# Optimization experiments

Measured on AMD Instinct MI355X. Metric: run time of the kernel, lower is better.

Reference implementation:

```python
import jax, jax.numpy as jnp
import numpy as np


def _coord(n):
    # grid-center coordinates in [-1, 1], matching make_coord
    r = 1.0 / n
    return -1.0 + r + 2.0 * r * jnp.arange(n, dtype=jnp.float32)


def setup_inputs() -> dict:
    key = jax.random.key(0)
    k1, k2, k3 = jax.random.split(key, 3)
    B, C, H, W = 4, 64, 128, 128
    n_feat = 64
    return {
        "x": jax.random.normal(k1, (B, C, H, W), jnp.float32),
        "W1": jax.random.normal(k2, (n_feat + 2, n_feat), jnp.float32) * 0.05,
        "b1": jnp.zeros((n_feat,), jnp.float32),
        "W2": jax.random.normal(k3, (n_feat, 3), jnp.float32) * 0.05,
        "b2": jnp.zeros((3,), jnp.float32),
        "out_size": 512,
    }


def reference(x, W1, b1, W2, b2, out_size):
    # radius == 1 -> F.unfold(x, 1, padding=0) is the identity, so x_unfold == x.
    B, C, H, W = x.shape
    Oh = Ow = out_size

    yc = _coord(Oh)  # [Oh] output-pixel-center y coords in [-1,1]
    xc = _coord(Ow)  # [Ow]

    # grid_sample(mode='nearest', align_corners=False): unnormalize then round
    # (nearbyint = round-half-to-even, matched by jnp.round). Coords are in
    # bounds, so clipping reproduces the in-range gather exactly.
    iy = jnp.clip(jnp.round(((yc + 1.0) * H - 1.0) * 0.5), 0, H - 1).astype(jnp.int32)
    ix = jnp.clip(jnp.round(((xc + 1.0) * W - 1.0) * 0.5), 0, W - 1).astype(jnp.int32)

    # nearest-neighbor gather of features: [B, C, Oh, Ow] -> [B, Oh, Ow, C]
    q_feat = jnp.transpose(x[:, :, iy, :][:, :, :, ix], (0, 2, 3, 1))

    # nearest input pixel-center coords (what grid-sampling in_coord returns)
    qy = -1.0 + (2.0 * iy.astype(jnp.float32) + 1.0) / H  # [Oh]
    qx = -1.0 + (2.0 * ix.astype(jnp.float32) + 1.0) / W  # [Ow]

    rel_y = (yc - qy) * H  # scaled by x.shape[-2]
    rel_x = (xc - qx) * W  # scaled by x.shape[-1]
    rel = jnp.stack(jnp.broadcast_arrays(rel_y[:, None], rel_x[None, :]), axis=-1)  # [Oh,Ow,2]

    inp = jnp.concatenate(
        [q_feat, jnp.broadcast_to(rel, (B, Oh, Ow, 2))], axis=-1
    )  # [B, Oh, Ow, C+2]

    h = jax.nn.relu(inp @ W1 + b1)   # [B, Oh, Ow, n_feat]
    pred = h @ W2 + b2               # [B, Oh, Ow, 3]
    return jnp.transpose(pred, (0, 3, 1, 2))  # [B, 3, Oh, Ow]
```

## Files before the change

kernel.cpp:

```cpp
#include <hip/hip_runtime.h>
#include <hip/hip_bf16.h>


#define PLANE (512 * 512)
#define PITCH 68

typedef __attribute__((ext_vector_type(8))) short  short8;
typedef __attribute__((ext_vector_type(4))) float  f32x4;

__device__ __forceinline__ short bf16_of(float f) {
    __hip_bfloat16 h = __float2bfloat16(f);
    return *reinterpret_cast<short*>(&h);
}

__global__ __launch_bounds__(512, 8) void mlp_interp_kernel(
    const float* __restrict__ x,
    const float* __restrict__ W1,
    const float* __restrict__ b1,
    const float* __restrict__ W2,
    const float* __restrict__ b2,
    float* __restrict__ out)
{
    __shared__ float fs[64][PITCH];

    const int tid = threadIdx.x;
    const int w   = tid >> 6;
    const int t   = tid & 63;

    const int blk  = blockIdx.x;
    const int lblk = blk & 1;
    const int k    = (blk >> 1) & 127;
    const int b    = blk >> 8;
    const int l0   = lblk * 64;

    {
        const int lane16 = t & 15;
        const int g      = t >> 4;
        const int mt     = w >> 1;
        const int nt0    = (w & 1) * 2;

        const float* xbase = x + (((size_t)(b * 64)) * 128 + k) * 128
                               + l0 + 16 * mt + lane16;
        short8 afrag[2];
        #pragma unroll
        for (int ks = 0; ks < 2; ++ks) {
            float tmp[8];
            #pragma unroll
            for (int i = 0; i < 8; ++i)
                tmp[i] = xbase[(size_t)(32 * ks + 8 * g + i) * 16384];
            #pragma unroll
            for (int i = 0; i < 8; ++i) afrag[ks][i] = bf16_of(tmp[i]);
        }

        #pragma unroll
        for (int ntp = 0; ntp < 2; ++ntp) {
            const int j = 16 * (nt0 + ntp) + lane16;
            short8 bfrag[2];
            #pragma unroll
            for (int ks = 0; ks < 2; ++ks) {
                float tmp[8];
                #pragma unroll
                for (int i = 0; i < 8; ++i)
                    tmp[i] = W1[(32 * ks + 8 * g + i) * 64 + j];
                #pragma unroll
                for (int i = 0; i < 8; ++i) bfrag[ks][i] = bf16_of(tmp[i]);
            }

            const float b1j = b1[j];
            f32x4 acc = {b1j, b1j, b1j, b1j};
            acc = __builtin_amdgcn_mfma_f32_16x16x32_bf16(afrag[0], bfrag[0], acc, 0, 0, 0);
            acc = __builtin_amdgcn_mfma_f32_16x16x32_bf16(afrag[1], bfrag[1], acc, 0, 0, 0);

            #pragma unroll
            for (int r = 0; r < 4; ++r)
                fs[16 * mt + 4 * g + r][j] = acc[r];
        }
    }
    __syncthreads();

    {
        const int ry = w >> 1;
        const int rh = w & 1;
        const float ay  = (2 * ry - 3) * 0.25f;
        const float ax0 = (2 * (2 * rh)     - 3) * 0.25f;
        const float ax1 = (2 * (2 * rh + 1) - 3) * 0.25f;

        const float* Ay = W1 + 64 * 64;
        const float* Ax = W1 + 65 * 64;

        float p00 = b2[0], p10 = b2[1], p20 = b2[2];
        float p01 = b2[0], p11 = b2[1], p21 = b2[2];

        #pragma unroll
        for (int q = 0; q < 4; ++q) {
            float f[16];
            #pragma unroll
            for (int u = 0; u < 4; ++u) {
                const float4 v = *(const float4*)&fs[t][16 * q + 4 * u];
                f[4*u] = v.x; f[4*u+1] = v.y; f[4*u+2] = v.z; f[4*u+3] = v.w;
            }
            #pragma unroll
            for (int i = 0; i < 16; ++i) {
                const int j = 16 * q + i;
                const float g2 = fmaf(ay, Ay[j], f[i]);
                const float h0 = fmaxf(fmaf(ax0, Ax[j], g2), 0.0f);
                const float h1 = fmaxf(fmaf(ax1, Ax[j], g2), 0.0f);
                const float w0 = W2[3*j + 0];
                const float w1 = W2[3*j + 1];
                const float w2 = W2[3*j + 2];
                p00 = fmaf(h0, w0, p00); p10 = fmaf(h0, w1, p10); p20 = fmaf(h0, w2, p20);
                p01 = fmaf(h1, w0, p01); p11 = fmaf(h1, w1, p11); p21 = fmaf(h1, w2, p21);
            }
        }

        const int oy  = 4 * k + ry;
        const int ox0 = (l0 + t) * 4 + 2 * rh;
        float* op = out + ((size_t)(b * 3) * 512 + oy) * 512 + ox0;
        float2 v0; v0.x = p00; v0.y = p01;
        float2 v1; v1.x = p10; v1.y = p11;
        float2 v2; v2.x = p20; v2.y = p21;
        *(float2*)(op)             = v0;
        *(float2*)(op +     PLANE) = v1;
        *(float2*)(op + 2 * PLANE) = v2;
    }
}

extern "C" void kernel_launch(void* const* d_in, const int* in_sizes, int n_in,
                              void* d_out, int out_size, void* d_ws, size_t ws_size,
                              hipStream_t stream) {
    const float* x  = (const float*)d_in[0];
    const float* W1 = (const float*)d_in[1];
    const float* b1 = (const float*)d_in[2];
    const float* W2 = (const float*)d_in[3];
    const float* b2 = (const float*)d_in[4];
    float* out = (float*)d_out;

    mlp_interp_kernel<<<1024, 512, 0, stream>>>(x, W1, b1, W2, b2, out);
}
```

Measured before the change: 84.75 us.

## Split block work into two 32-pixel halves with double-buffered shared staging

Each block now runs 256 threads and processes its 64 input pixels in two halves, using two shared buffers. The MFMA feature projection for the second half is issued before the per-pixel MLP for the first half, so global loads and matrix work can overlap the scalar stage. This aims to hide load latency and reduce one-barrier serialization. In exchange, each block has half the threads and does twice the sequential work, and a second barrier is added.

```diff
diff --git a/kernel.cpp b/kernel.cpp
--- a/kernel.cpp
+++ b/kernel.cpp
@@ -13,7 +13,105 @@
     return *reinterpret_cast<short*>(&h);
 }
 
-__global__ __launch_bounds__(512, 8) void mlp_interp_kernel(
+__device__ __forceinline__ void stage1(const float* __restrict__ xb,
+                                       const float* __restrict__ W1,
+                                       const float* __restrict__ b1,
+                                       int w, int t, float (&fs)[32][PITCH]) {
+    const int lane16 = t & 15;
+    const int g      = t >> 4;
+    const int mt     = w >> 1;
+    const int nt0    = (w & 1) * 2;
+
+    const float* xbase = xb + 16 * mt + lane16;
+    short8 afrag[2];
+    #pragma unroll
+    for (int ks = 0; ks < 2; ++ks) {
+        float tmp[8];
+        #pragma unroll
+        for (int i = 0; i < 8; ++i)
+            tmp[i] = xbase[(size_t)(32 * ks + 8 * g + i) * 16384];
+        #pragma unroll
+        for (int i = 0; i < 8; ++i) afrag[ks][i] = bf16_of(tmp[i]);
+    }
+
+    #pragma unroll
+    for (int ntp = 0; ntp < 2; ++ntp) {
+        const int j = 16 * (nt0 + ntp) + lane16;
+        short8 bfrag[2];
+        #pragma unroll
+        for (int ks = 0; ks < 2; ++ks) {
+            float tmp[8];
+            #pragma unroll
+            for (int i = 0; i < 8; ++i)
+                tmp[i] = W1[(32 * ks + 8 * g + i) * 64 + j];
+            #pragma unroll
+            for (int i = 0; i < 8; ++i) bfrag[ks][i] = bf16_of(tmp[i]);
+        }
+
+        const float b1j = b1[j];
+        f32x4 acc = {b1j, b1j, b1j, b1j};
+        acc = __builtin_amdgcn_mfma_f32_16x16x32_bf16(afrag[0], bfrag[0], acc, 0, 0, 0);
+        acc = __builtin_amdgcn_mfma_f32_16x16x32_bf16(afrag[1], bfrag[1], acc, 0, 0, 0);
+
+        #pragma unroll
+        for (int r = 0; r < 4; ++r)
+            fs[16 * mt + 4 * g + r][j] = acc[r];
+    }
+}
+
+__device__ __forceinline__ void stage2(const float* __restrict__ W1,
+                                       const float* __restrict__ W2,
+                                       const float* __restrict__ b2,
+                                       int w, int t, int k, int b, int l0t,
+                                       const float (&fs)[32][PITCH],
+                                       float* __restrict__ out) {
+    const int p  = t & 31;
+    const int rh = t >> 5;
+    const int ry = w;
+    const float ay  = (2 * ry - 3) * 0.25f;
+    const float ax0 = (2 * (2 * rh)     - 3) * 0.25f;
+    const float ax1 = (2 * (2 * rh + 1) - 3) * 0.25f;
+
+    const float* Ay = W1 + 64 * 64;
+    const float* Ax = W1 + 65 * 64;
+
+    float p00 = b2[0], p10 = b2[1], p20 = b2[2];
+    float p01 = b2[0], p11 = b2[1], p21 = b2[2];
+
+    #pragma unroll
+    for (int q = 0; q < 4; ++q) {
+        float f[16];
+        #pragma unroll
+        for (int u = 0; u < 4; ++u) {
+            const float4 v = *(const float4*)&fs[p][16 * q + 4 * u];
+            f[4*u] = v.x; f[4*u+1] = v.y; f[4*u+2] = v.z; f[4*u+3] = v.w;
+        }
+        #pragma unroll
+        for (int i = 0; i < 16; ++i) {
+            const int j = 16 * q + i;
+            const float g2 = fmaf(ay, Ay[j], f[i]);
+            const float h0 = fmaxf(fmaf(ax0, Ax[j], g2), 0.0f);
+            const float h1 = fmaxf(fmaf(ax1, Ax[j], g2), 0.0f);
+            const float w0 = W2[3*j + 0];
+            const float w1 = W2[3*j + 1];
+            const float w2 = W2[3*j + 2];
+            p00 = fmaf(h0, w0, p00); p10 = fmaf(h0, w1, p10); p20 = fmaf(h0, w2, p20);
+            p01 = fmaf(h1, w0, p01); p11 = fmaf(h1, w1, p11); p21 = fmaf(h1, w2, p21);
+        }
+    }
+
+    const int oy  = 4 * k + ry;
+    const int ox0 = (l0t + p) * 4 + 2 * rh;
+    float* op = out + ((size_t)(b * 3) * 512 + oy) * 512 + ox0;
+    float2 v0; v0.x = p00; v0.y = p01;
+    float2 v1; v1.x = p10; v1.y = p11;
+    float2 v2; v2.x = p20; v2.y = p21;
+    *(float2*)(op)             = v0;
+    *(float2*)(op +     PLANE) = v1;
+    *(float2*)(op + 2 * PLANE) = v2;
+}
+
+__global__ __launch_bounds__(256, 4) void mlp_interp_kernel(
     const float* __restrict__ x,
     const float* __restrict__ W1,
     const float* __restrict__ b1,
@@ -21,7 +119,8 @@
     const float* __restrict__ b2,
     float* __restrict__ out)
 {
-    __shared__ float fs[64][PITCH];
+    __shared__ float fs0[32][PITCH];
+    __shared__ float fs1[32][PITCH];
 
     const int tid = threadIdx.x;
     const int w   = tid >> 6;
@@ -33,96 +132,16 @@
     const int b    = blk >> 8;
     const int l0   = lblk * 64;
 
-    {
-        const int lane16 = t & 15;
-        const int g      = t >> 4;
-        const int mt     = w >> 1;
-        const int nt0    = (w & 1) * 2;
+    const float* xb = x + (((size_t)(b * 64)) * 128 + k) * 128;
 
-        const float* xbase = x + (((size_t)(b * 64)) * 128 + k) * 128
-                               + l0 + 16 * mt + lane16;
-        short8 afrag[2];
-        #pragma unroll
-        for (int ks = 0; ks < 2; ++ks) {
-            float tmp[8];
-            #pragma unroll
-            for (int i = 0; i < 8; ++i)
-                tmp[i] = xbase[(size_t)(32 * ks + 8 * g + i) * 16384];
-            #pragma unroll
-            for (int i = 0; i < 8; ++i) afrag[ks][i] = bf16_of(tmp[i]);
-        }
-
-        #pragma unroll
-        for (int ntp = 0; ntp < 2; ++ntp) {
-            const int j = 16 * (nt0 + ntp) + lane16;
-            short8 bfrag[2];
-            #pragma unroll
-            for (int ks = 0; ks < 2; ++ks) {
-                float tmp[8];
-                #pragma unroll
-                for (int i = 0; i < 8; ++i)
-                    tmp[i] = W1[(32 * ks + 8 * g + i) * 64 + j];
-                #pragma unroll
-                for (int i = 0; i < 8; ++i) bfrag[ks][i] = bf16_of(tmp[i]);
-            }
-
-            const float b1j = b1[j];
-            f32x4 acc = {b1j, b1j, b1j, b1j};
-            acc = __builtin_amdgcn_mfma_f32_16x16x32_bf16(afrag[0], bfrag[0], acc, 0, 0, 0);
-            acc = __builtin_amdgcn_mfma_f32_16x16x32_bf16(afrag[1], bfrag[1], acc, 0, 0, 0);
-
-            #pragma unroll
-            for (int r = 0; r < 4; ++r)
-                fs[16 * mt + 4 * g + r][j] = acc[r];
-        }
-    }
+    stage1(xb + l0, W1, b1, w, t, fs0);
     __syncthreads();
 
-    {
-        const int ry = w >> 1;
-        const int rh = w & 1;
-        const float ay  = (2 * ry - 3) * 0.25f;
-        const float ax0 = (2 * (2 * rh)     - 3) * 0.25f;
-        const float ax1 = (2 * (2 * rh + 1) - 3) * 0.25f;
+    stage1(xb + l0 + 32, W1, b1, w, t, fs1);
+    stage2(W1, W2, b2, w, t, k, b, l0, fs0, out);
+    __syncthreads();
 
-        const float* Ay = W1 + 64 * 64;
-        const float* Ax = W1 + 65 * 64;
-
-        float p00 = b2[0], p10 = b2[1], p20 = b2[2];
-        float p01 = b2[0], p11 = b2[1], p21 = b2[2];
-
-        #pragma unroll
-        for (int q = 0; q < 4; ++q) {
-            float f[16];
-            #pragma unroll
-            for (int u = 0; u < 4; ++u) {
-                const float4 v = *(const float4*)&fs[t][16 * q + 4 * u];
-                f[4*u] = v.x; f[4*u+1] = v.y; f[4*u+2] = v.z; f[4*u+3] = v.w;
-            }
-            #pragma unroll
-            for (int i = 0; i < 16; ++i) {
-                const int j = 16 * q + i;
-                const float g2 = fmaf(ay, Ay[j], f[i]);
-                const float h0 = fmaxf(fmaf(ax0, Ax[j], g2), 0.0f);
-                const float h1 = fmaxf(fmaf(ax1, Ax[j], g2), 0.0f);
-                const float w0 = W2[3*j + 0];
-                const float w1 = W2[3*j + 1];
-                const float w2 = W2[3*j + 2];
-                p00 = fmaf(h0, w0, p00); p10 = fmaf(h0, w1, p10); p20 = fmaf(h0, w2, p20);
-                p01 = fmaf(h1, w0, p01); p11 = fmaf(h1, w1, p11); p21 = fmaf(h1, w2, p21);
-            }
-        }
-
-        const int oy  = 4 * k + ry;
-        const int ox0 = (l0 + t) * 4 + 2 * rh;
-        float* op = out + ((size_t)(b * 3) * 512 + oy) * 512 + ox0;
-        float2 v0; v0.x = p00; v0.y = p01;
-        float2 v1; v1.x = p10; v1.y = p11;
-        float2 v2; v2.x = p20; v2.y = p21;
-        *(float2*)(op)             = v0;
-        *(float2*)(op +     PLANE) = v1;
-        *(float2*)(op + 2 * PLANE) = v2;
-    }
+    stage2(W1, W2, b2, w, t, k, b, l0 + 32, fs1, out);
 }
 
 extern "C" void kernel_launch(void* const* d_in, const int* in_sizes, int n_in,
@@ -135,5 +154,5 @@
     const float* b2 = (const float*)d_in[4];
     float* out = (float*)d_out;
 
-    mlp_interp_kernel<<<1024, 512, 0, stream>>>(x, W1, b1, W2, b2, out);
+    mlp_interp_kernel<<<1024, 256, 0, stream>>>(x, W1, b1, W2, b2, out);
 }
```

After: 94.03 us. 1.11x slower.

## Restructure work split so each wave owns a 16-pixel strip without block sync

Applied to the files above, without the earlier changes.

Each wave now computes the full 64-wide first-layer MFMA for its own 16 input pixels and then evaluates all 4x4 output sub-pixels for those pixels, writing float4 rows. Because each wave touches only its own shared-memory slice, the block-wide barrier is removed. Blocks shrink to 128 threads and the grid doubles. The intent is to drop the sync and widen the output stores, at the cost of each wave loading all W1 B-fragments (four instead of two) and holding more accumulators per thread.

```diff
diff --git a/kernel.cpp b/kernel.cpp
--- a/kernel.cpp
+++ b/kernel.cpp
@@ -13,7 +13,7 @@
     return *reinterpret_cast<short*>(&h);
 }
 
-__global__ __launch_bounds__(512, 8) void mlp_interp_kernel(
+__global__ __launch_bounds__(128, 4) void mlp_interp_kernel(
     const float* __restrict__ x,
     const float* __restrict__ W1,
     const float* __restrict__ b1,
@@ -21,26 +21,23 @@
     const float* __restrict__ b2,
     float* __restrict__ out)
 {
-    __shared__ float fs[64][PITCH];
+    __shared__ float fs[2][16][PITCH];
 
     const int tid = threadIdx.x;
     const int w   = tid >> 6;
     const int t   = tid & 63;
 
-    const int blk  = blockIdx.x;
-    const int lblk = blk & 1;
-    const int k    = (blk >> 1) & 127;
-    const int b    = blk >> 8;
-    const int l0   = lblk * 64;
+    const int blk   = blockIdx.x;
+    const int strip = blk & 3;
+    const int k     = (blk >> 2) & 127;
+    const int b     = blk >> 9;
+    const int l0    = strip * 32 + w * 16;
+
+    const int lane16 = t & 15;
+    const int g      = t >> 4;
 
     {
-        const int lane16 = t & 15;
-        const int g      = t >> 4;
-        const int mt     = w >> 1;
-        const int nt0    = (w & 1) * 2;
-
-        const float* xbase = x + (((size_t)(b * 64)) * 128 + k) * 128
-                               + l0 + 16 * mt + lane16;
+        const float* xbase = x + (((size_t)(b * 64)) * 128 + k) * 128 + l0 + lane16;
         short8 afrag[2];
         #pragma unroll
         for (int ks = 0; ks < 2; ++ks) {
@@ -53,8 +50,8 @@
         }
 
         #pragma unroll
-        for (int ntp = 0; ntp < 2; ++ntp) {
-            const int j = 16 * (nt0 + ntp) + lane16;
+        for (int nt = 0; nt < 4; ++nt) {
+            const int j = 16 * nt + lane16;
             short8 bfrag[2];
             #pragma unroll
             for (int ks = 0; ks < 2; ++ks) {
@@ -73,55 +70,60 @@
 
             #pragma unroll
             for (int r = 0; r < 4; ++r)
-                fs[16 * mt + 4 * g + r][j] = acc[r];
+                fs[w][4 * g + r][j] = acc[r];
         }
     }
-    __syncthreads();
 
     {
-        const int ry = w >> 1;
-        const int rh = w & 1;
-        const float ay  = (2 * ry - 3) * 0.25f;
-        const float ax0 = (2 * (2 * rh)     - 3) * 0.25f;
-        const float ax1 = (2 * (2 * rh + 1) - 3) * 0.25f;
+        const int px = lane16;
+        const int ry = g;
+        const float ay = (2 * ry - 3) * 0.25f;
+        const float ax0 = -0.75f, ax1 = -0.25f, ax2 = 0.25f, ax3 = 0.75f;
 
         const float* Ay = W1 + 64 * 64;
         const float* Ax = W1 + 65 * 64;
 
-        float p00 = b2[0], p10 = b2[1], p20 = b2[2];
-        float p01 = b2[0], p11 = b2[1], p21 = b2[2];
+        float p0c0 = b2[0], p0c1 = b2[1], p0c2 = b2[2];
+        float p1c0 = b2[0], p1c1 = b2[1], p1c2 = b2[2];
+        float p2c0 = b2[0], p2c1 = b2[1], p2c2 = b2[2];
+        float p3c0 = b2[0], p3c1 = b2[1], p3c2 = b2[2];
 
         #pragma unroll
         for (int q = 0; q < 4; ++q) {
             float f[16];
             #pragma unroll
             for (int u = 0; u < 4; ++u) {
-                const float4 v = *(const float4*)&fs[t][16 * q + 4 * u];
+                const float4 v = *(const float4*)&fs[w][px][16 * q + 4 * u];
                 f[4*u] = v.x; f[4*u+1] = v.y; f[4*u+2] = v.z; f[4*u+3] = v.w;
             }
             #pragma unroll
             for (int i = 0; i < 16; ++i) {
                 const int j = 16 * q + i;
                 const float g2 = fmaf(ay, Ay[j], f[i]);
-                const float h0 = fmaxf(fmaf(ax0, Ax[j], g2), 0.0f);
-                const float h1 = fmaxf(fmaf(ax1, Ax[j], g2), 0.0f);
+                const float axj = Ax[j];
+                const float h0 = fmaxf(fmaf(ax0, axj, g2), 0.0f);
+                const float h1 = fmaxf(fmaf(ax1, axj, g2), 0.0f);
+                const float h2 = fmaxf(fmaf(ax2, axj, g2), 0.0f);
+                const float h3 = fmaxf(fmaf(ax3, axj, g2), 0.0f);
                 const float w0 = W2[3*j + 0];
                 const float w1 = W2[3*j + 1];
                 const float w2 = W2[3*j + 2];
-                p00 = fmaf(h0, w0, p00); p10 = fmaf(h0, w1, p10); p20 = fmaf(h0, w2, p20);
-                p01 = fmaf(h1, w0, p01); p11 = fmaf(h1, w1, p11); p21 = fmaf(h1, w2, p21);
+                p0c0 = fmaf(h0, w0, p0c0); p0c1 = fmaf(h0, w1, p0c1); p0c2 = fmaf(h0, w2, p0c2);
+                p1c0 = fmaf(h1, w0, p1c0); p1c1 = fmaf(h1, w1, p1c1); p1c2 = fmaf(h1, w2, p1c2);
+                p2c0 = fmaf(h2, w0, p2c0); p2c1 = fmaf(h2, w1, p2c1); p2c2 = fmaf(h2, w2, p2c2);
+                p3c0 = fmaf(h3, w0, p3c0); p3c1 = fmaf(h3, w1, p3c1); p3c2 = fmaf(h3, w2, p3c2);
             }
         }
 
         const int oy  = 4 * k + ry;
-        const int ox0 = (l0 + t) * 4 + 2 * rh;
+        const int ox0 = (l0 + px) * 4;
         float* op = out + ((size_t)(b * 3) * 512 + oy) * 512 + ox0;
-        float2 v0; v0.x = p00; v0.y = p01;
-        float2 v1; v1.x = p10; v1.y = p11;
-        float2 v2; v2.x = p20; v2.y = p21;
-        *(float2*)(op)             = v0;
-        *(float2*)(op +     PLANE) = v1;
-        *(float2*)(op + 2 * PLANE) = v2;
+        float4 v0; v0.x = p0c0; v0.y = p1c0; v0.z = p2c0; v0.w = p3c0;
+        float4 v1; v1.x = p0c1; v1.y = p1c1; v1.z = p2c1; v1.w = p3c1;
+        float4 v2; v2.x = p0c2; v2.y = p1c2; v2.z = p2c2; v2.w = p3c2;
+        *(float4*)(op)             = v0;
+        *(float4*)(op +     PLANE) = v1;
+        *(float4*)(op + 2 * PLANE) = v2;
     }
 }
 
@@ -135,5 +137,5 @@
     const float* b2 = (const float*)d_in[4];
     float* out = (float*)d_out;
 
-    mlp_interp_kernel<<<1024, 512, 0, stream>>>(x, W1, b1, W2, b2, out);
+    mlp_interp_kernel<<<2048, 128, 0, stream>>>(x, W1, b1, W2, b2, out);
 }
```

After: 84.42 us. About the same (-0.4%).
